# Performance work log

Hardware: AMD Instinct MI355X
Metric: run time of the kernel (lower is better)

## Reference

```python
import jax, jax.numpy as jnp
import numpy as np

TOP_K = 2
B, S, H, I, E = 1, 2048, 1024, 4096, 8


def setup_inputs() -> dict:
    key = jax.random.key(0)
    k1, k2, k3, k4 = jax.random.split(key, 4)
    x = jax.random.normal(k1, (B, S, H), dtype=jnp.float32)
    gate_w = jax.random.normal(k2, (E, H), dtype=jnp.float32)
    w1 = jax.random.normal(k3, (E, I, H), dtype=jnp.float32)
    w2 = jax.random.normal(k4, (E, H, I), dtype=jnp.float32)
    return {"x": x, "gate_w": gate_w, "w1": w1, "w2": w2}


def reference(x, gate_w, w1, w2):
    b, s, h = x.shape
    xf = x.reshape(-1, h)                      # [T, H]
    T = xf.shape[0]
    logits = xf @ gate_w.T                     # [T, E]
    probs = jax.nn.softmax(logits, axis=-1)
    wts, idx = jax.lax.top_k(probs, TOP_K)     # [T, k]
    wts = wts / jnp.sum(wts, axis=-1, keepdims=True)
    # combine[t, e] = routing weight of expert e for token t (0 if not selected)
    combine = jnp.zeros((T, w1.shape[0]), dtype=x.dtype)
    combine = combine.at[jnp.arange(T)[:, None], idx].add(wts)
    # dense dispatch: every expert processes every token, masked/weighted by combine
    hid = jax.nn.silu(jnp.einsum('th,eih->tei', xf, w1))   # [T, E, I]
    y = jnp.einsum('tei,ehi->teh', hid, w2)                # [T, E, H]
    out = jnp.einsum('teh,te->th', y, combine)             # [T, H]
    return out.reshape(b, s, h)
```

## Files before the change

kernel.cpp:

```cpp
#include <hip/hip_runtime.h>
#include <stdint.h>

#define TT 2048
#define HH 1024
#define II 4096
#define EE 8
#define KS 4

typedef __attribute__((ext_vector_type(4))) float floatx4;
typedef __attribute__((ext_vector_type(8))) __bf16 bf16x8;

__device__ __forceinline__ unsigned short f2bf(float f) {
  union { float f; unsigned u; } v; v.f = f;
  return (unsigned short)((v.u + 0x7FFFu + ((v.u >> 16) & 1u)) >> 16);
}

__device__ __forceinline__ void async_ld16(const void* g, void* l) {
  __builtin_amdgcn_global_load_lds(
      (__attribute__((address_space(1))) void*)g,
      (__attribute__((address_space(3))) void*)l, 16, 0, 0);
}

__global__ __launch_bounds__(256) void k_gating(
    const float* __restrict__ x, const float* __restrict__ gw,
    unsigned short* __restrict__ xb, int* __restrict__ sel_e,
    float* __restrict__ sel_w, int* __restrict__ counts) {
  int t = blockIdx.x;
  int tid = threadIdx.x;
  floatx4 xv = ((const floatx4*)(x + (size_t)t * HH))[tid];
  ushort4 xo;
  xo.x = f2bf(xv.x); xo.y = f2bf(xv.y); xo.z = f2bf(xv.z); xo.w = f2bf(xv.w);
  ((ushort4*)(xb + (size_t)t * HH))[tid] = xo;

  float part[EE];
#pragma unroll
  for (int e = 0; e < EE; e++) {
    floatx4 g = ((const floatx4*)(gw + e * HH))[tid];
    part[e] = xv.x * g.x + xv.y * g.y + xv.z * g.z + xv.w * g.w;
  }
#pragma unroll
  for (int e = 0; e < EE; e++) {
    float v = part[e];
#pragma unroll
    for (int off = 32; off > 0; off >>= 1) v += __shfl_down(v, off, 64);
    part[e] = v;
  }
  __shared__ float red[4][EE];
  int wave = tid >> 6;
  if ((tid & 63) == 0) {
#pragma unroll
    for (int e = 0; e < EE; e++) red[wave][e] = part[e];
  }
  __syncthreads();
  if (tid == 0) {
    float lg[EE];
#pragma unroll
    for (int e = 0; e < EE; e++)
      lg[e] = red[0][e] + red[1][e] + red[2][e] + red[3][e];
    int e0 = 0;
#pragma unroll
    for (int e = 1; e < EE; e++) if (lg[e] > lg[e0]) e0 = e;
    int e1 = (e0 == 0) ? 1 : 0;
#pragma unroll
    for (int e = 0; e < EE; e++) if (e != e0 && lg[e] > lg[e1]) e1 = e;
    float w0 = 1.f / (1.f + expf(lg[e1] - lg[e0]));
    sel_e[t * 2] = e0; sel_e[t * 2 + 1] = e1;
    sel_w[t * 2] = w0; sel_w[t * 2 + 1] = 1.f - w0;
    atomicAdd(&counts[e0], 1);
    atomicAdd(&counts[e1], 1);
  }
}

__global__ __launch_bounds__(256) void k_fill(
    const int* __restrict__ counts, const int* __restrict__ sel_e,
    const float* __restrict__ sel_w, int* __restrict__ bases,
    int* __restrict__ row_token, float* __restrict__ row_w,
    int* __restrict__ inv_slot) {
  __shared__ int lb[EE];
  __shared__ int lc[EE];
  int tid = threadIdx.x;
  if (tid == 0) {
    int s = 0;
    for (int e = 0; e < EE; e++) { lb[e] = s; s += counts[e]; }
  }
  if (tid < EE) lc[tid] = 0;
  __syncthreads();
  for (int p = tid; p < TT * 2; p += 256) {
    int e = sel_e[p];
    int slot = lb[e] + atomicAdd(&lc[e], 1);
    row_token[slot] = p >> 1;
    row_w[slot] = sel_w[p];
    inv_slot[p] = slot;
  }
  __syncthreads();
  if (tid < EE) bases[tid] = lb[tid];
}

__global__ __launch_bounds__(256) void k_gemm1(
    const unsigned short* __restrict__ xb,
    const float* __restrict__ w1,
    unsigned short* __restrict__ hid,
    const int* __restrict__ counts, const int* __restrict__ bases,
    const int* __restrict__ row_token) {
  const int e = blockIdx.z;
  const int count = counts[e];
  const int m0 = blockIdx.y * 128;
  if (m0 >= count) return;
  const int n0 = blockIdx.x * 128;
  const int base = bases[e];

  __shared__ __align__(16) unsigned short Smem[128 * 32 * 2];
  unsigned short* As = Smem;
  unsigned short* Bs = Smem + 128 * 32;

  const int tid = threadIdx.x;
  const int lane = tid & 63;
  const int wave = tid >> 6;
  const int wm = (wave & 1) * 64;
  const int wn = (wave >> 1) * 64;
  const int quad = lane >> 4;
  const int l16 = lane & 15;

  const int rA0 = tid >> 2;
  const int rA1 = rA0 + 64;
  const int cc = (tid & 3) * 8;

  int g0 = m0 + rA0; if (g0 > count - 1) g0 = count - 1;
  int g1 = m0 + rA1; if (g1 > count - 1) g1 = count - 1;
  const unsigned short* aS0 = xb + (size_t)row_token[base + g0] * HH + cc;
  const unsigned short* aS1 = xb + (size_t)row_token[base + g1] * HH + cc;
  const float* wp = w1 + (size_t)e * II * HH;
  const float* bp0 = wp + (size_t)(n0 + rA0) * HH + cc;
  const float* bp1 = wp + (size_t)(n0 + rA1) * HH + cc;

  unsigned short* lA0 = As + tid * 8;
  unsigned short* lA1 = As + tid * 8 + 2048;
  unsigned short* lB0 = Bs + tid * 8;
  unsigned short* lB1 = Bs + tid * 8 + 2048;

  const floatx4 fz = {0.f, 0.f, 0.f, 0.f};
  floatx4 acc[4][4];
#pragma unroll
  for (int i = 0; i < 4; i++)
#pragma unroll
    for (int j = 0; j < 4; j++) acc[i][j] = fz;

  floatx4 f0a = *(const floatx4*)(bp0);
  floatx4 f0b = *(const floatx4*)(bp0 + 4);
  floatx4 f1a = *(const floatx4*)(bp1);
  floatx4 f1b = *(const floatx4*)(bp1 + 4);

  for (int k0 = 0; k0 < HH; k0 += 32) {
    bf16x8 wv0, wv1;
#pragma unroll
    for (int j = 0; j < 4; j++) {
      wv0[j] = (__bf16)f0a[j]; wv0[j + 4] = (__bf16)f0b[j];
      wv1[j] = (__bf16)f1a[j]; wv1[j + 4] = (__bf16)f1b[j];
    }
    *(bf16x8*)lB0 = wv0;
    *(bf16x8*)lB1 = wv1;
    async_ld16(aS0 + k0, lA0);
    async_ld16(aS1 + k0, lA1);
    __syncthreads();
    if (k0 + 32 < HH) {
      f0a = *(const floatx4*)(bp0 + k0 + 32);
      f0b = *(const floatx4*)(bp0 + k0 + 36);
      f1a = *(const floatx4*)(bp1 + k0 + 32);
      f1b = *(const floatx4*)(bp1 + k0 + 36);
    }
    bf16x8 af[4], bfr[4];
#pragma unroll
    for (int i = 0; i < 4; i++) {
      af[i]  = *(const bf16x8*)(As + (wm + i * 16 + l16) * 32 + quad * 8);
      bfr[i] = *(const bf16x8*)(Bs + (wn + i * 16 + l16) * 32 + quad * 8);
    }
#pragma unroll
    for (int i = 0; i < 4; i++)
#pragma unroll
      for (int j = 0; j < 4; j++)
        acc[i][j] = __builtin_amdgcn_mfma_f32_16x16x32_bf16(af[i], bfr[j], acc[i][j], 0, 0, 0);
    __syncthreads();
  }

  unsigned short* Sl = Smem + wave * (16 * 72);
#pragma unroll
  for (int i = 0; i < 4; i++) {
#pragma unroll
    for (int r = 0; r < 4; r++) {
      const int row16 = quad * 4 + r;
#pragma unroll
      for (int j = 0; j < 4; j++) {
        float z = acc[i][j][r];
        Sl[row16 * 72 + l16 + 16 * j] = f2bf(z / (1.f + __expf(-z)));
      }
    }
#pragma unroll
    for (int half = 0; half < 2; half++) {
      const int row16 = (lane >> 3) + 8 * half;
      const int m = wm + i * 16 + row16;
      if (m0 + m < count) {
        bf16x8 v = *(const bf16x8*)(Sl + row16 * 72 + (lane & 7) * 8);
        *(bf16x8*)(hid + (size_t)(base + m0 + m) * II + n0 + wn + (lane & 7) * 8) = v;
      }
    }
  }
}

__global__ __launch_bounds__(256) void k_gemm2(
    const unsigned short* __restrict__ hid,
    const float* __restrict__ w2,
    float* __restrict__ yp,
    const int* __restrict__ counts, const int* __restrict__ bases) {
  const int e = blockIdx.z;
  const int count = counts[e];
  const int m0 = blockIdx.y * 128;
  if (m0 >= count) return;
  const int nt = blockIdx.x & 7;
  const int ks = blockIdx.x >> 3;
  const int n0 = nt * 128;
  const int base = bases[e];

  __shared__ __align__(16) unsigned short Smem2[128 * 32 * 2];
  unsigned short* As = Smem2;
  unsigned short* Bs = Smem2 + 128 * 32;

  const int tid = threadIdx.x;
  const int lane = tid & 63;
  const int wave = tid >> 6;
  const int wm = (wave & 1) * 64;
  const int wn = (wave >> 1) * 64;
  const int quad = lane >> 4;
  const int l16 = lane & 15;

  const int rA0 = tid >> 2;
  const int rA1 = rA0 + 64;
  const int cc = (tid & 3) * 8;

  int g0 = m0 + rA0; if (g0 > count - 1) g0 = count - 1;
  int g1 = m0 + rA1; if (g1 > count - 1) g1 = count - 1;
  const unsigned short* aS0 = hid + (size_t)(base + g0) * II + cc;
  const unsigned short* aS1 = hid + (size_t)(base + g1) * II + cc;
  const float* wp = w2 + (size_t)e * HH * II;
  const float* bp0 = wp + (size_t)(n0 + rA0) * II + cc;
  const float* bp1 = wp + (size_t)(n0 + rA1) * II + cc;

  unsigned short* lA0 = As + tid * 8;
  unsigned short* lA1 = As + tid * 8 + 2048;
  unsigned short* lB0 = Bs + tid * 8;
  unsigned short* lB1 = Bs + tid * 8 + 2048;

  const floatx4 fz = {0.f, 0.f, 0.f, 0.f};
  floatx4 acc[4][4];
#pragma unroll
  for (int i = 0; i < 4; i++)
#pragma unroll
    for (int j = 0; j < 4; j++) acc[i][j] = fz;

  const int kbeg = ks * (II / KS);
  const int kend = kbeg + II / KS;

  floatx4 f0a = *(const floatx4*)(bp0 + kbeg);
  floatx4 f0b = *(const floatx4*)(bp0 + kbeg + 4);
  floatx4 f1a = *(const floatx4*)(bp1 + kbeg);
  floatx4 f1b = *(const floatx4*)(bp1 + kbeg + 4);

  for (int k0 = kbeg; k0 < kend; k0 += 32) {
    bf16x8 wv0, wv1;
#pragma unroll
    for (int j = 0; j < 4; j++) {
      wv0[j] = (__bf16)f0a[j]; wv0[j + 4] = (__bf16)f0b[j];
      wv1[j] = (__bf16)f1a[j]; wv1[j + 4] = (__bf16)f1b[j];
    }
    *(bf16x8*)lB0 = wv0;
    *(bf16x8*)lB1 = wv1;
    async_ld16(aS0 + k0, lA0);
    async_ld16(aS1 + k0, lA1);
    __syncthreads();
    if (k0 + 32 < kend) {
      f0a = *(const floatx4*)(bp0 + k0 + 32);
      f0b = *(const floatx4*)(bp0 + k0 + 36);
      f1a = *(const floatx4*)(bp1 + k0 + 32);
      f1b = *(const floatx4*)(bp1 + k0 + 36);
    }
    bf16x8 af[4], bfr[4];
#pragma unroll
    for (int i = 0; i < 4; i++) {
      af[i]  = *(const bf16x8*)(As + (wm + i * 16 + l16) * 32 + quad * 8);
      bfr[i] = *(const bf16x8*)(Bs + (wn + i * 16 + l16) * 32 + quad * 8);
    }
#pragma unroll
    for (int i = 0; i < 4; i++)
#pragma unroll
      for (int j = 0; j < 4; j++)
        acc[i][j] = __builtin_amdgcn_mfma_f32_16x16x32_bf16(af[i], bfr[j], acc[i][j], 0, 0, 0);
    __syncthreads();
  }

#pragma unroll
  for (int i = 0; i < 4; i++) {
#pragma unroll
    for (int r = 0; r < 4; r++) {
      const int m = wm + i * 16 + quad * 4 + r;
      if (m0 + m < count) {
        float* op = yp + ((size_t)ks * (TT * 2) + base + m0 + m) * HH + n0 + wn + l16;
#pragma unroll
        for (int j = 0; j < 4; j++) op[j * 16] = acc[i][j][r];
      }
    }
  }
}

__global__ __launch_bounds__(256) void k_combine(
    const float* __restrict__ yp, const int* __restrict__ inv_slot,
    const float* __restrict__ sel_w, float* __restrict__ out) {
  const int t = blockIdx.x;
  const int tid = threadIdx.x;
  const int s0 = inv_slot[2 * t];
  const int s1 = inv_slot[2 * t + 1];
  const float w0 = sel_w[2 * t];
  const float w1 = sel_w[2 * t + 1];
  floatx4 a = {0.f, 0.f, 0.f, 0.f};
  floatx4 b = {0.f, 0.f, 0.f, 0.f};
#pragma unroll
  for (int ks = 0; ks < KS; ks++) {
    a += ((const floatx4*)(yp + ((size_t)ks * (TT * 2) + s0) * HH))[tid];
    b += ((const floatx4*)(yp + ((size_t)ks * (TT * 2) + s1) * HH))[tid];
  }
  floatx4 v = w0 * a + w1 * b;
  ((floatx4*)(out + (size_t)t * HH))[tid] = v;
}

extern "C" void kernel_launch(void* const* d_in, const int* in_sizes, int n_in,
                              void* d_out, int out_size, void* d_ws, size_t ws_size,
                              hipStream_t stream) {
  const float* x  = (const float*)d_in[0];
  const float* gw = (const float*)d_in[1];
  const float* w1 = (const float*)d_in[2];
  const float* w2 = (const float*)d_in[3];
  float* out = (float*)d_out;

  char* ws = (char*)d_ws;
  size_t off = 0;
  auto take = [&](size_t n) -> char* {
    char* p = ws + off;
    off += (n + 255) & ~(size_t)255;
    return p;
  };
  unsigned short* xb  = (unsigned short*)take((size_t)TT * HH * 2);
  unsigned short* hid = (unsigned short*)take((size_t)TT * 2 * II * 2);
  float* yp = (float*)take((size_t)KS * (TT * 2) * HH * 4);
  int*   counts    = (int*)take(EE * 4);
  int*   bases     = (int*)take(EE * 4);
  int*   row_token = (int*)take((size_t)TT * 2 * 4);
  float* row_w     = (float*)take((size_t)TT * 2 * 4);
  int*   sel_e     = (int*)take((size_t)TT * 2 * 4);
  float* sel_w     = (float*)take((size_t)TT * 2 * 4);
  int*   inv_slot  = (int*)take((size_t)TT * 2 * 4);
  if (off > ws_size) return;

  hipMemsetAsync(counts, 0, EE * 4, stream);

  k_gating<<<TT, 256, 0, stream>>>(x, gw, xb, sel_e, sel_w, counts);
  k_fill<<<1, 256, 0, stream>>>(counts, sel_e, sel_w, bases, row_token, row_w, inv_slot);
  k_gemm1<<<dim3(II / 128, 16, EE), 256, 0, stream>>>(xb, w1, hid, counts, bases, row_token);
  k_gemm2<<<dim3(8 * KS, 16, EE), 256, 0, stream>>>(hid, w2, yp, counts, bases);
  k_combine<<<TT, 256, 0, stream>>>(yp, inv_slot, sel_w, out);
}
```

Before: 468.9 us.

## Stage fp32 weights directly into LDS asynchronously with XOR swizzle

Both grouped GEMMs now load the fp32 weight tiles straight into shared memory with async global-to-LDS loads, rather than prefetching them into registers, converting, and storing bf16. The bf16 conversion moves to after the LDS read, and A/B tiles use XOR swizzling to avoid bank conflicts. Launch bounds request three blocks per CU. This frees registers and the store path, but doubles B-tile LDS footprint and read traffic and removes the register prefetch overlap, so the global load latency is now only covered by the sync.

```diff
diff --git a/kernel.cpp b/kernel.cpp
--- a/kernel.cpp
+++ b/kernel.cpp
@@ -96,7 +96,8 @@
   if (tid < EE) bases[tid] = lb[tid];
 }
 
-__global__ __launch_bounds__(256) void k_gemm1(
+
+__global__ __launch_bounds__(256, 3) void k_gemm1(
     const unsigned short* __restrict__ xb,
     const float* __restrict__ w1,
     unsigned short* __restrict__ hid,
@@ -109,9 +110,8 @@
   const int n0 = blockIdx.x * 128;
   const int base = bases[e];
 
-  __shared__ __align__(16) unsigned short Smem[128 * 32 * 2];
-  unsigned short* As = Smem;
-  unsigned short* Bs = Smem + 128 * 32;
+  __shared__ __align__(16) unsigned short As[128 * 32];
+  __shared__ __align__(16) float Bs[128 * 32];
 
   const int tid = threadIdx.x;
   const int lane = tid & 63;
@@ -122,21 +122,30 @@
   const int l16 = lane & 15;
 
   const int rA0 = tid >> 2;
-  const int rA1 = rA0 + 64;
-  const int cc = (tid & 3) * 8;
-
+  const int cA = (((tid & 3) ^ ((rA0 >> 1) & 3))) * 8;
   int g0 = m0 + rA0; if (g0 > count - 1) g0 = count - 1;
-  int g1 = m0 + rA1; if (g1 > count - 1) g1 = count - 1;
-  const unsigned short* aS0 = xb + (size_t)row_token[base + g0] * HH + cc;
-  const unsigned short* aS1 = xb + (size_t)row_token[base + g1] * HH + cc;
-  const float* wp = w1 + (size_t)e * II * HH;
-  const float* bp0 = wp + (size_t)(n0 + rA0) * HH + cc;
-  const float* bp1 = wp + (size_t)(n0 + rA1) * HH + cc;
-
+  int g1 = m0 + rA0 + 64; if (g1 > count - 1) g1 = count - 1;
+  const unsigned short* aS0 = xb + (size_t)row_token[base + g0] * HH + cA;
+  const unsigned short* aS1 = xb + (size_t)row_token[base + g1] * HH + cA;
   unsigned short* lA0 = As + tid * 8;
   unsigned short* lA1 = As + tid * 8 + 2048;
-  unsigned short* lB0 = Bs + tid * 8;
-  unsigned short* lB1 = Bs + tid * 8 + 2048;
+
+  const int rB = tid >> 3;
+  const int cB = ((lane & 7) ^ (lane >> 3)) * 4;
+  const float* bS = w1 + (size_t)e * II * HH + (size_t)(n0 + rB) * HH + cB;
+  float* lB = Bs + tid * 4;
+
+  const unsigned short* aF[4];
+  const float* bF0[4];
+  const float* bF1[4];
+#pragma unroll
+  for (int i = 0; i < 4; i++) {
+    int R = wm + i * 16 + l16;
+    aF[i] = As + R * 32 + (quad ^ ((R >> 1) & 3)) * 8;
+    int Rb = wn + i * 16 + l16;
+    bF0[i] = Bs + Rb * 32 + ((2 * quad) ^ (Rb & 7)) * 4;
+    bF1[i] = Bs + Rb * 32 + ((2 * quad + 1) ^ (Rb & 7)) * 4;
+  }
 
   const floatx4 fz = {0.f, 0.f, 0.f, 0.f};
   floatx4 acc[4][4];
@@ -145,34 +154,25 @@
 #pragma unroll
     for (int j = 0; j < 4; j++) acc[i][j] = fz;
 
-  floatx4 f0a = *(const floatx4*)(bp0);
-  floatx4 f0b = *(const floatx4*)(bp0 + 4);
-  floatx4 f1a = *(const floatx4*)(bp1);
-  floatx4 f1b = *(const floatx4*)(bp1 + 4);
-
   for (int k0 = 0; k0 < HH; k0 += 32) {
-    bf16x8 wv0, wv1;
-#pragma unroll
-    for (int j = 0; j < 4; j++) {
-      wv0[j] = (__bf16)f0a[j]; wv0[j + 4] = (__bf16)f0b[j];
-      wv1[j] = (__bf16)f1a[j]; wv1[j + 4] = (__bf16)f1b[j];
-    }
-    *(bf16x8*)lB0 = wv0;
-    *(bf16x8*)lB1 = wv1;
     async_ld16(aS0 + k0, lA0);
     async_ld16(aS1 + k0, lA1);
+#pragma unroll
+    for (int i = 0; i < 4; i++)
+      async_ld16(bS + (size_t)(32 * i) * HH + k0, lB + i * 1024);
     __syncthreads();
-    if (k0 + 32 < HH) {
-      f0a = *(const floatx4*)(bp0 + k0 + 32);
-      f0b = *(const floatx4*)(bp0 + k0 + 36);
-      f1a = *(const floatx4*)(bp1 + k0 + 32);
-      f1b = *(const floatx4*)(bp1 + k0 + 36);
-    }
     bf16x8 af[4], bfr[4];
 #pragma unroll
-    for (int i = 0; i < 4; i++) {
-      af[i]  = *(const bf16x8*)(As + (wm + i * 16 + l16) * 32 + quad * 8);
-      bfr[i] = *(const bf16x8*)(Bs + (wn + i * 16 + l16) * 32 + quad * 8);
+    for (int i = 0; i < 4; i++) af[i] = *(const bf16x8*)aF[i];
+#pragma unroll
+    for (int j = 0; j < 4; j++) {
+      floatx4 u0 = *(const floatx4*)bF0[j];
+      floatx4 u1 = *(const floatx4*)bF1[j];
+#pragma unroll
+      for (int t = 0; t < 4; t++) {
+        bfr[j][t] = (__bf16)u0[t];
+        bfr[j][t + 4] = (__bf16)u1[t];
+      }
     }
 #pragma unroll
     for (int i = 0; i < 4; i++)
@@ -182,7 +182,7 @@
     __syncthreads();
   }
 
-  unsigned short* Sl = Smem + wave * (16 * 72);
+  unsigned short* Sl = ((unsigned short*)Bs) + wave * (16 * 72);
 #pragma unroll
   for (int i = 0; i < 4; i++) {
 #pragma unroll
@@ -206,7 +206,7 @@
   }
 }
 
-__global__ __launch_bounds__(256) void k_gemm2(
+__global__ __launch_bounds__(256, 3) void k_gemm2(
     const unsigned short* __restrict__ hid,
     const float* __restrict__ w2,
     float* __restrict__ yp,
@@ -220,9 +220,8 @@
   const int n0 = nt * 128;
   const int base = bases[e];
 
-  __shared__ __align__(16) unsigned short Smem2[128 * 32 * 2];
-  unsigned short* As = Smem2;
-  unsigned short* Bs = Smem2 + 128 * 32;
+  __shared__ __align__(16) unsigned short As[128 * 32];
+  __shared__ __align__(16) float Bs[128 * 32];
 
   const int tid = threadIdx.x;
   const int lane = tid & 63;
@@ -233,21 +232,30 @@
   const int l16 = lane & 15;
 
   const int rA0 = tid >> 2;
-  const int rA1 = rA0 + 64;
-  const int cc = (tid & 3) * 8;
-
+  const int cA = (((tid & 3) ^ ((rA0 >> 1) & 3))) * 8;
   int g0 = m0 + rA0; if (g0 > count - 1) g0 = count - 1;
-  int g1 = m0 + rA1; if (g1 > count - 1) g1 = count - 1;
-  const unsigned short* aS0 = hid + (size_t)(base + g0) * II + cc;
-  const unsigned short* aS1 = hid + (size_t)(base + g1) * II + cc;
-  const float* wp = w2 + (size_t)e * HH * II;
-  const float* bp0 = wp + (size_t)(n0 + rA0) * II + cc;
-  const float* bp1 = wp + (size_t)(n0 + rA1) * II + cc;
-
+  int g1 = m0 + rA0 + 64; if (g1 > count - 1) g1 = count - 1;
+  const unsigned short* aS0 = hid + (size_t)(base + g0) * II + cA;
+  const unsigned short* aS1 = hid + (size_t)(base + g1) * II + cA;
   unsigned short* lA0 = As + tid * 8;
   unsigned short* lA1 = As + tid * 8 + 2048;
-  unsigned short* lB0 = Bs + tid * 8;
-  unsigned short* lB1 = Bs + tid * 8 + 2048;
+
+  const int rB = tid >> 3;
+  const int cB = ((lane & 7) ^ (lane >> 3)) * 4;
+  const float* bS = w2 + (size_t)e * HH * II + (size_t)(n0 + rB) * II + cB;
+  float* lB = Bs + tid * 4;
+
+  const unsigned short* aF[4];
+  const float* bF0[4];
+  const float* bF1[4];
+#pragma unroll
+  for (int i = 0; i < 4; i++) {
+    int R = wm + i * 16 + l16;
+    aF[i] = As + R * 32 + (quad ^ ((R >> 1) & 3)) * 8;
+    int Rb = wn + i * 16 + l16;
+    bF0[i] = Bs + Rb * 32 + ((2 * quad) ^ (Rb & 7)) * 4;
+    bF1[i] = Bs + Rb * 32 + ((2 * quad + 1) ^ (Rb & 7)) * 4;
+  }
 
   const floatx4 fz = {0.f, 0.f, 0.f, 0.f};
   floatx4 acc[4][4];
@@ -258,35 +266,25 @@
 
   const int kbeg = ks * (II / KS);
   const int kend = kbeg + II / KS;
-
-  floatx4 f0a = *(const floatx4*)(bp0 + kbeg);
-  floatx4 f0b = *(const floatx4*)(bp0 + kbeg + 4);
-  floatx4 f1a = *(const floatx4*)(bp1 + kbeg);
-  floatx4 f1b = *(const floatx4*)(bp1 + kbeg + 4);
-
   for (int k0 = kbeg; k0 < kend; k0 += 32) {
-    bf16x8 wv0, wv1;
-#pragma unroll
-    for (int j = 0; j < 4; j++) {
-      wv0[j] = (__bf16)f0a[j]; wv0[j + 4] = (__bf16)f0b[j];
-      wv1[j] = (__bf16)f1a[j]; wv1[j + 4] = (__bf16)f1b[j];
-    }
-    *(bf16x8*)lB0 = wv0;
-    *(bf16x8*)lB1 = wv1;
     async_ld16(aS0 + k0, lA0);
     async_ld16(aS1 + k0, lA1);
+#pragma unroll
+    for (int i = 0; i < 4; i++)
+      async_ld16(bS + (size_t)(32 * i) * II + k0, lB + i * 1024);
     __syncthreads();
-    if (k0 + 32 < kend) {
-      f0a = *(const floatx4*)(bp0 + k0 + 32);
-      f0b = *(const floatx4*)(bp0 + k0 + 36);
-      f1a = *(const floatx4*)(bp1 + k0 + 32);
-      f1b = *(const floatx4*)(bp1 + k0 + 36);
-    }
     bf16x8 af[4], bfr[4];
 #pragma unroll
-    for (int i = 0; i < 4; i++) {
-      af[i]  = *(const bf16x8*)(As + (wm + i * 16 + l16) * 32 + quad * 8);
-      bfr[i] = *(const bf16x8*)(Bs + (wn + i * 16 + l16) * 32 + quad * 8);
+    for (int i = 0; i < 4; i++) af[i] = *(const bf16x8*)aF[i];
+#pragma unroll
+    for (int j = 0; j < 4; j++) {
+      floatx4 u0 = *(const floatx4*)bF0[j];
+      floatx4 u1 = *(const floatx4*)bF1[j];
+#pragma unroll
+      for (int t = 0; t < 4; t++) {
+        bfr[j][t] = (__bf16)u0[t];
+        bfr[j][t + 4] = (__bf16)u1[t];
+      }
     }
 #pragma unroll
     for (int i = 0; i < 4; i++)
```

Measured after the change: 476.9 us. About the same (+1.7%).
